# Kernel optimization log

Hardware: AMD Instinct MI355X
Metric: run time of the kernel (lower is better)

Reference implementation:

```python
import jax, jax.numpy as jnp
import numpy as np

GRID = 128      # voxel grid extent per axis
NUM_BATCH = 4
N_PER = 25000   # points per scene (unique voxels)
C = 128
K = 32          # number of classes in probs
HEADS = 8
SCALE = 1.0


def setup_inputs() -> dict:
    key = jax.random.key(0)
    ks = jax.random.split(key, 12)
    N = NUM_BATCH * N_PER
    # unique voxel coordinates per scene (submanifold conv assumes no duplicate sites)
    coords_list = []
    for b in range(NUM_BATCH):
        flat = jax.random.permutation(jax.random.fold_in(ks[0], b), GRID ** 3)[:N_PER]
        xyz = jnp.stack([flat // (GRID * GRID), (flat // GRID) % GRID, flat % GRID], axis=1)
        bcol = jnp.full((N_PER, 1), b)
        coords_list.append(jnp.concatenate([bcol, xyz], axis=1))
    coords = jnp.concatenate(coords_list, axis=0).astype(jnp.int32)  # [N,4] = (b,x,y,z)
    feats = jax.random.normal(ks[1], (N, C), jnp.float32)
    probs = jax.random.normal(ks[2], (N, K), jnp.float32)
    conv_w = jax.random.normal(ks[3], (27, C, C), jnp.float32) * (1.0 / np.sqrt(27 * C))
    bn_gamma = 1.0 + 0.1 * jax.random.normal(ks[4], (C,), jnp.float32)
    bn_beta = 0.1 * jax.random.normal(ks[5], (C,), jnp.float32)
    in_proj_w = jax.random.normal(ks[6], (3 * C, C), jnp.float32) / np.sqrt(C)
    in_proj_b = 0.01 * jax.random.normal(ks[7], (3 * C,), jnp.float32)
    out_proj_w = jax.random.normal(ks[8], (C, C), jnp.float32) / np.sqrt(C)
    out_proj_b = 0.01 * jax.random.normal(ks[9], (C,), jnp.float32)
    bottleneck_w = jax.random.normal(ks[10], (C, 2 * C), jnp.float32) / np.sqrt(2 * C)
    return {"feats": feats, "probs": probs, "conv_w": conv_w, "bn_gamma": bn_gamma,
            "bn_beta": bn_beta, "in_proj_w": in_proj_w, "in_proj_b": in_proj_b,
            "out_proj_w": out_proj_w, "out_proj_b": out_proj_b,
            "bottleneck_w": bottleneck_w, "coords": coords, "batch_size": NUM_BATCH}


def _subm_conv3x3(feats, coords, conv_w, batch_size):
    """Submanifold 3x3x3 sparse conv: outputs only at active sites, gathering active neighbors."""
    N = feats.shape[0]
    b, xyz = coords[:, 0], coords[:, 1:]
    grid = jnp.full((batch_size, GRID, GRID, GRID), -1, jnp.int32)
    grid = grid.at[b, xyz[:, 0], xyz[:, 1], xyz[:, 2]].set(jnp.arange(N, dtype=jnp.int32))
    out = jnp.zeros((N, conv_w.shape[-1]), feats.dtype)
    kidx = 0
    for dx in (-1, 0, 1):
        for dy in (-1, 0, 1):
            for dz in (-1, 0, 1):
                nb = xyz + jnp.array([dx, dy, dz], jnp.int32)
                inb = jnp.all((nb >= 0) & (nb < GRID), axis=1)
                nbc = jnp.clip(nb, 0, GRID - 1)
                j = grid[b, nbc[:, 0], nbc[:, 1], nbc[:, 2]]
                ok = inb & (j >= 0)
                g = jnp.where(ok[:, None], feats[jnp.maximum(j, 0)], 0.0)
                out = out + g @ conv_w[kidx]
                kidx += 1
    return out


def _forward(feats, probs, conv_w, bn_gamma, bn_beta, in_proj_w, in_proj_b,
             out_proj_w, out_proj_b, bottleneck_w, coords, batch_size):
    N, Cc = feats.shape
    dh = Cc // HEADS
    b = coords[:, 0]
    # transform_input: SubMConv3d -> BatchNorm1d (batch stats) -> ReLU
    x = _subm_conv3x3(feats, coords, conv_w, batch_size)
    mu = jnp.mean(x, axis=0)
    var = jnp.var(x, axis=0)
    x = jax.nn.relu((x - mu) * jax.lax.rsqrt(var + 1e-5) * bn_gamma + bn_beta)
    # SpatialGatherModule: per-scene softmax over points, soft-weighted context [B,K,C]
    m = b[None, :] == jnp.arange(batch_size, dtype=b.dtype)[:, None]          # [B,N]
    neg = jnp.finfo(x.dtype).min
    z = jnp.where(m[:, :, None], (SCALE * probs)[None], neg)                  # [B,N,K]
    w = jax.nn.softmax(z, axis=1)
    ctx = jnp.einsum('bnk,nc->bkc', w, x)                                     # [B,K,C]
    # per-scene MultiheadAttention (unbatched): query = points, key/value = context
    Wq, Wk, Wv = in_proj_w[:Cc], in_proj_w[Cc:2 * Cc], in_proj_w[2 * Cc:]
    bq, bk, bv = in_proj_b[:Cc], in_proj_b[Cc:2 * Cc], in_proj_b[2 * Cc:]
    q = ((x @ Wq.T + bq) * (dh ** -0.5)).reshape(N, HEADS, dh)
    kh = (ctx @ Wk.T + bk).reshape(batch_size, -1, HEADS, dh)
    vh = (ctx @ Wv.T + bv).reshape(batch_size, -1, HEADS, dh)
    scores = jnp.einsum('nhd,bkhd->nbhk', q, kh)
    scores = scores[jnp.arange(N), b]                                         # [N,H,K] pick own scene
    attn = jax.nn.softmax(scores, axis=-1)
    o = jnp.einsum('nhk,bkhd->nbhd', attn, vh)[jnp.arange(N), b]              # [N,H,dh]
    attn_out = o.reshape(N, Cc) @ out_proj_w.T + out_proj_b
    # torch code aliases feats with inputs.features, so the in-place scatter makes
    # both halves of the concat equal to attn_out (literal forward semantics)
    y = jnp.concatenate([attn_out, attn_out], axis=1) @ bottleneck_w.T
    return y


def reference(feats, probs, conv_w, bn_gamma, bn_beta, in_proj_w, in_proj_b,
              out_proj_w, out_proj_b, bottleneck_w, coords, batch_size):
    return _forward(feats, probs, conv_w, bn_gamma, bn_beta, in_proj_w, in_proj_b,
                    out_proj_w, out_proj_b, bottleneck_w, coords, batch_size)
```

## Files before the change

### kernel.cpp

```cpp
#include <hip/hip_runtime.h>
#include <hip/hip_bf16.h>

typedef __attribute__((ext_vector_type(8))) short short8;
typedef __attribute__((ext_vector_type(4))) float floatx4;

#define NB 4
#define GRIDD 128
#define GRID3 (128*128*128)
#define C 128
#define KSLOT 32
#define CTX_BPB 256
#define DEN_BLK 1024
#define STAT_BLK 1024
#define PCAP 8192

static __device__ __forceinline__ unsigned short f2bf(float f){
  unsigned u = __builtin_bit_cast(unsigned, f);
  unsigned r = (u + 0x7FFFu + ((u >> 16) & 1u)) >> 16;
  return (unsigned short)r;
}
static __device__ __forceinline__ float bf2f(unsigned short h){
  unsigned u = ((unsigned)h) << 16;
  return __builtin_bit_cast(float, u);
}

__global__ void prepk(const float* __restrict__ feats, const float* __restrict__ convw,
                      const float* __restrict__ inw,
                      unsigned short* __restrict__ Fb, unsigned short* __restrict__ Wt,
                      unsigned short* __restrict__ Wq, unsigned short* __restrict__ WkvT,
                      long total1)
{
  const long stride = (long)gridDim.x * blockDim.x;
  const long i0 = (long)blockIdx.x * blockDim.x + threadIdx.x;
  const long q4 = total1 >> 2;
  const float4* f4 = reinterpret_cast<const float4*>(feats);
  ushort4* fb4 = reinterpret_cast<ushort4*>(Fb);
  for (long i = i0; i < q4; i += stride){
    const float4 v = f4[i];
    ushort4 o; o.x = f2bf(v.x); o.y = f2bf(v.y); o.z = f2bf(v.z); o.w = f2bf(v.w);
    fb4[i] = o;
  }
  for (long i = i0; i < 27L*C*C; i += stride){
    long k = i >> 14; long r = (i >> 7) & 127; long c = i & 127;
    Wt[i] = f2bf(convw[(k << 14) + (c << 7) + r]);
  }
  for (long i = i0; i < C*C; i += stride) Wq[i] = f2bf(inw[i]);
  for (long i = i0; i < 2L*C*C; i += stride){
    long which = i >> 14, rem = i & 16383, ii = rem >> 7, cout = rem & 127;
    WkvT[i] = f2bf(inw[((1 + which) << 14) + (cout << 7) + ii]);
  }
}

__global__ __launch_bounds__(128) void w2k(const float* __restrict__ bw,
                                           const float* __restrict__ outw,
                                           const float* __restrict__ outb,
                                           unsigned short* __restrict__ W2b,
                                           float* __restrict__ b2){
  const int o = blockIdx.x, i = threadIdx.x;
  __shared__ float wcf[128];
  __shared__ float red[128];
  const float w_i = bw[(size_t)o*256 + i] + bw[(size_t)o*256 + 128 + i];
  wcf[i] = w_i;
  red[i] = w_i * outb[i];
  __syncthreads();
  float acc = 0.f;
  #pragma unroll 8
  for (int j = 0; j < 128; j++) acc = fmaf(wcf[j], outw[j*128 + i], acc);
  W2b[o*128 + i] = f2bf(acc);
  for (int s = 64; s > 0; s >>= 1){
    if (i < s) red[i] += red[i + s];
    __syncthreads();
  }
  if (i == 0) b2[o] = red[0];
}

__global__ void scatterk(const int* __restrict__ coords, int* __restrict__ gh, int N){
  int p = blockIdx.x * 256 + threadIdx.x;
  if (p < N){
    int4 cr = *reinterpret_cast<const int4*>(coords + (size_t)p * 4);
    gh[(((cr.x*GRIDD + cr.y)*GRIDD + cr.z)*GRIDD) + cr.w] = p;
  }
}

__global__ __launch_bounds__(256) void pairk(const int* __restrict__ coords,
                                             const int* __restrict__ gh,
                                             int2* __restrict__ pairs,
                                             int* __restrict__ gcnt, int N){
  __shared__ int wcnt[4][27];
  __shared__ int woff[4][27];
  const int t = threadIdx.x, wave = t >> 6, lane = t & 63;
  const int p = blockIdx.x * 256 + t;
  const bool active = p < N;
  int4 cr = make_int4(0, 0, 0, 0);
  if (active) cr = *reinterpret_cast<const int4*>(coords + (size_t)p * 4);
  const int b = cr.x, x = cr.y, y = cr.z, z = cr.w;
  int jl[27];
  #pragma unroll
  for (int k = 0; k < 27; k++){
    jl[k] = -1;
    if (k == 13) continue;
    if (active){
      const int dx = k / 9 - 1, dy = (k / 3) % 3 - 1, dz = k % 3 - 1;
      const int nx = x + dx, ny = y + dy, nz = z + dz;
      if (((unsigned)nx < 128u) & ((unsigned)ny < 128u) & ((unsigned)nz < 128u)){
        const int gi = ((((b << 7) + nx) << 7) + ny) * GRIDD + nz;
        const int jj = gh[gi];
        if ((unsigned)jj < (unsigned)N){
          const int4 cj = *reinterpret_cast<const int4*>(coords + (size_t)jj * 4);
          if (cj.x == b && cj.y == nx && cj.z == ny && cj.w == nz) jl[k] = jj;
        }
      }
    }
  }
  #pragma unroll
  for (int k = 0; k < 27; k++){
    const unsigned long long m = __ballot(jl[k] >= 0);
    if (lane == 0) wcnt[wave][k] = (int)__popcll(m);
  }
  __syncthreads();
  if (t < 27){
    const int c0 = wcnt[0][t], c1 = wcnt[1][t], c2 = wcnt[2][t], c3 = wcnt[3][t];
    const int tot = c0 + c1 + c2 + c3;
    int gb = 0;
    if (t != 13 && tot > 0) gb = atomicAdd(&gcnt[t], tot);
    woff[0][t] = gb;
    woff[1][t] = gb + c0;
    woff[2][t] = gb + c0 + c1;
    woff[3][t] = gb + c0 + c1 + c2;
  }
  __syncthreads();
  const unsigned long long ltm = ((unsigned long long)1 << lane) - 1;
  #pragma unroll
  for (int k = 0; k < 27; k++){
    if (k == 13) continue;
    const unsigned long long m = __ballot(jl[k] >= 0);
    if (jl[k] >= 0){
      const int slot = woff[wave][k] + (int)__popcll(m & ltm);
      if (slot < PCAP) pairs[(size_t)k * PCAP + slot] = make_int2(p, jl[k]);
    }
  }
}

__global__ __launch_bounds__(256) void scatk(
    const unsigned short* __restrict__ F, const unsigned short* __restrict__ Wt,
    const int2* __restrict__ pairs, const int* __restrict__ gcnt,
    float* __restrict__ X, int N)
{
  __shared__ unsigned short wl[128 * 136];
  const int k = (blockIdx.x < 13) ? blockIdx.x : blockIdx.x + 1;
  const int t = threadIdx.x;
  const unsigned short* wg = Wt + (size_t)k * C * C;
  for (int idx = t; idx < 128 * 16; idx += 256){
    const int row = idx >> 4, seg = idx & 15;
    *reinterpret_cast<short8*>(&wl[row * 136 + seg * 8]) =
        *reinterpret_cast<const short8*>(wg + row * 128 + seg * 8);
  }
  __syncthreads();
  const int cnt = min(gcnt[k], PCAP);
  const int nch = (cnt + 15) >> 4;
  const int wave = t >> 6, lane = t & 63, lo = lane & 15, hi = lane >> 4;
  for (int c = blockIdx.y * 4 + wave; c < nch; c += 32 * 4){
    const int pidx = c * 16 + lo;
    const bool pv = pidx < cnt;
    const int2 pr = pv ? pairs[(size_t)k * PCAP + pidx] : make_int2(0, 0);
    const unsigned short* frow = F + (size_t)pr.y * C;
    short8 a[4];
    #pragma unroll
    for (int kc = 0; kc < 4; kc++){
      a[kc] = *reinterpret_cast<const short8*>(frow + kc * 32 + hi * 8);
      if (!pv) a[kc] = (short8){0,0,0,0,0,0,0,0};
    }
    floatx4 acc[8];
    #pragma unroll
    for (int i = 0; i < 8; i++) acc[i] = (floatx4){0.f,0.f,0.f,0.f};
    #pragma unroll
    for (int kc = 0; kc < 4; kc++){
      const int koff = kc * 32 + hi * 8;
      #pragma unroll
      for (int ct = 0; ct < 8; ct++){
        const short8 b = *reinterpret_cast<const short8*>(&wl[(ct*16 + lo) * 136 + koff]);
        acc[ct] = __builtin_amdgcn_mfma_f32_16x16x32_bf16(a[kc], b, acc[ct], 0, 0, 0);
      }
    }
    #pragma unroll
    for (int i2 = 0; i2 < 4; i2++){
      const int src = hi * 4 + i2;
      const int row = __shfl(pr.x, src);
      if (c * 16 + src < cnt){
        #pragma unroll
        for (int ct = 0; ct < 8; ct++)
          atomicAdd(&X[(size_t)row * C + ct * 16 + lo], acc[ct][i2]);
      }
    }
  }
}

__global__ __launch_bounds__(256) void denomk(const float* __restrict__ probs,
                                              const int* __restrict__ coords,
                                              float* __restrict__ dpart, int N){
  const int t = threadIdx.x, k = t & 31, rh = t >> 5;
  float a0 = 0.f, a1 = 0.f, a2 = 0.f, a3 = 0.f;
  for (int r = blockIdx.x * 8 + rh; r < N; r += DEN_BLK * 8){
    const int b = coords[(size_t)r * 4];
    const float e = __expf(probs[(size_t)r * 32 + k]);
    a0 += (b == 0) ? e : 0.f;
    a1 += (b == 1) ? e : 0.f;
    a2 += (b == 2) ? e : 0.f;
    a3 += (b == 3) ? e : 0.f;
  }
  __shared__ float ls[8][128];
  ls[rh][0*32 + k] = a0; ls[rh][1*32 + k] = a1;
  ls[rh][2*32 + k] = a2; ls[rh][3*32 + k] = a3;
  __syncthreads();
  if (t < 128){
    float s = 0.f;
    #pragma unroll
    for (int j = 0; j < 8; j++) s += ls[j][t];
    dpart[(size_t)blockIdx.x * 128 + t] = s;
  }
}

__global__ __launch_bounds__(256) void statsk(const float* __restrict__ X,
                                              float* __restrict__ spgs, int N){
  const int t = threadIdx.x, c4 = t & 31, rg = t >> 5;
  float s0=0.f,s1=0.f,s2=0.f,s3=0.f, q0=0.f,q1=0.f,q2=0.f,q3=0.f;
  for (int r = blockIdx.x * 8 + rg; r < N; r += STAT_BLK * 8){
    const float4 v = *reinterpret_cast<const float4*>(X + (size_t)r * C + c4 * 4);
    s0 += v.x; s1 += v.y; s2 += v.z; s3 += v.w;
    q0 = fmaf(v.x, v.x, q0); q1 = fmaf(v.y, v.y, q1);
    q2 = fmaf(v.z, v.z, q2); q3 = fmaf(v.w, v.w, q3);
  }
  __shared__ float ls[256][4], lq[256][4];
  ls[t][0]=s0; ls[t][1]=s1; ls[t][2]=s2; ls[t][3]=s3;
  lq[t][0]=q0; lq[t][1]=q1; lq[t][2]=q2; lq[t][3]=q3;
  __syncthreads();
  if (t < 32){
    float as[4]={0.f,0.f,0.f,0.f}, aq[4]={0.f,0.f,0.f,0.f};
    #pragma unroll
    for (int g = 0; g < 8; g++){
      #pragma unroll
      for (int j = 0; j < 4; j++){ as[j] += ls[g*32 + t][j]; aq[j] += lq[g*32 + t][j]; }
    }
    #pragma unroll
    for (int j = 0; j < 4; j++){
      spgs[(size_t)blockIdx.x * 256 + t*4 + j] = as[j];
      spgs[(size_t)blockIdx.x * 256 + 128 + t*4 + j] = aq[j];
    }
  }
}

__global__ __launch_bounds__(128) void reduk(const float* __restrict__ pgs,
                                             const float* __restrict__ dpart,
                                             float* __restrict__ gsum,
                                             float* __restrict__ gsq,
                                             float* __restrict__ denom){
  const int which = blockIdx.x, slice = blockIdx.y, t = threadIdx.x;
  float s = 0.f;
  if (which < 2){
    const float* src = pgs + which * 128 + t;
    for (int j = slice; j < STAT_BLK; j += 8) s += src[(size_t)j * 256];
    atomicAdd((which ? gsq : gsum) + t, s);
  } else {
    const float* src = dpart + t;
    for (int j = slice; j < DEN_BLK; j += 8) s += src[(size_t)j * 128];
    atomicAdd(denom + t, s);
  }
}

__global__ void finalizek(const float* __restrict__ sums, const float* __restrict__ sumsq,
                          const float* __restrict__ gamma, const float* __restrict__ beta,
                          const float* __restrict__ denom,
                          float* __restrict__ scalev, float* __restrict__ shiftv,
                          float* __restrict__ invden, int N){
  const int t = threadIdx.x;
  const float invN = 1.f / (float)N;
  const float mu = sums[t] * invN;
  const float var = sumsq[t] * invN - mu * mu;
  const float sc = gamma[t] * rsqrtf(var + 1e-5f);
  scalev[t] = sc;
  shiftv[t] = beta[t] - mu * sc;
  invden[t] = 1.f / denom[t];
}

__global__ __launch_bounds__(256) void ctx2k(const float* __restrict__ Xm,
                                             const float* __restrict__ probs,
                                             const float* __restrict__ scalev,
                                             const float* __restrict__ shiftv,
                                             float* __restrict__ pbuf, int NPER){
  __shared__ float xL[32 * 128];
  __shared__ float pe[32 * 32];
  __shared__ float red[2 * KSLOT * C];
  const int blk = blockIdx.x;
  const int b = blk >> 8, j = blk & 255;
  const int rows = (NPER + CTX_BPB - 1) / CTX_BPB;
  const int r0 = j * rows;
  const int r1 = min(r0 + rows, NPER);
  const int t = threadIdx.x, c = t & 127, rh = t >> 7;
  const float sc = scalev[c], sh = shiftv[c];
  float acc[KSLOT];
  #pragma unroll
  for (int k = 0; k < KSLOT; k++) acc[k] = 0.f;

  for (int base = r0; base < r1; base += 32){
    __syncthreads();
    #pragma unroll
    for (int i = 0; i < 4; i++){
      const int idx = i * 256 + t;
      const int r = idx >> 5, c4 = idx & 31;
      const int rr = base + r;
      float4 v = make_float4(0.f, 0.f, 0.f, 0.f);
      if (rr < r1) v = *reinterpret_cast<const float4*>(Xm + ((size_t)b * NPER + rr) * C + c4 * 4);
      *reinterpret_cast<float4*>(&xL[r * 128 + c4 * 4]) = v;
    }
    {
      const int r = t >> 3, k4 = t & 7;
      const int rr = base + r;
      float4 v = make_float4(0.f, 0.f, 0.f, 0.f);
      if (rr < r1){
        const float4 pv = *reinterpret_cast<const float4*>(probs + ((size_t)b * NPER + rr) * 32 + k4 * 4);
        v.x = __expf(pv.x); v.y = __expf(pv.y); v.z = __expf(pv.z); v.w = __expf(pv.w);
      }
      *reinterpret_cast<float4*>(&pe[r * 32 + k4 * 4]) = v;
    }
    __syncthreads();
    const int rend = min(32, r1 - base);
    for (int r = rh; r < rend; r += 2){
      const float xv = fmaxf(fmaf(xL[r * 128 + c], sc, sh), 0.f);
      const float4* wr = reinterpret_cast<const float4*>(&pe[r * 32]);
      #pragma unroll
      for (int kq = 0; kq < 8; kq++){
        const float4 w4 = wr[kq];
        acc[kq*4+0] = fmaf(w4.x, xv, acc[kq*4+0]);
        acc[kq*4+1] = fmaf(w4.y, xv, acc[kq*4+1]);
        acc[kq*4+2] = fmaf(w4.z, xv, acc[kq*4+2]);
        acc[kq*4+3] = fmaf(w4.w, xv, acc[kq*4+3]);
      }
    }
  }
  __syncthreads();
  #pragma unroll
  for (int k = 0; k < KSLOT; k++) red[(rh * KSLOT + k) * C + c] = acc[k];
  __syncthreads();
  float* dst = pbuf + (size_t)blk * KSLOT * C;
  for (int i = t; i < KSLOT * C; i += 256) dst[i] = red[i] + red[KSLOT * C + i];
}

__global__ __launch_bounds__(256) void kvk(const float* __restrict__ pbuf,
                                           const float* __restrict__ invden,
                                           const unsigned short* __restrict__ WkvT,
                                           const float* __restrict__ inb,
                                           float* __restrict__ kh, float* __restrict__ vh){
  __shared__ float rowp[2][C];
  __shared__ float row[C];
  const int bk = blockIdx.x;
  const int b = bk >> 5, k = bk & 31;
  const int t = threadIdx.x, c = t & 127, jh = t >> 7;
  float s = 0.f;
  for (int j = jh; j < CTX_BPB; j += 2)
    s += pbuf[((size_t)(b * CTX_BPB + j) * KSLOT + k) * C + c];
  rowp[jh][c] = s;
  __syncthreads();
  if (t < C) row[t] = (rowp[0][t] + rowp[1][t]) * invden[b * KSLOT + k];
  __syncthreads();
  const int which = t >> 7;
  const unsigned short* W = WkvT + (size_t)which * C * C;
  float acc = inb[(1 + which) * C + c];
  #pragma unroll 8
  for (int i = 0; i < C; i++) acc = fmaf(row[i], bf2f(W[i * C + c]), acc);
  (which ? vh : kh)[(size_t)bk * C + c] = acc;
}

__global__ __launch_bounds__(256) void gemm128(
    const unsigned short* __restrict__ A, const unsigned short* __restrict__ W,
    const float* __restrict__ bias, float scale,
    float* __restrict__ outF, unsigned short* __restrict__ outB, int N)
{
  const int tid = threadIdx.x;
  const int wave = tid >> 6, lane = tid & 63;
  const int rbase = blockIdx.x * 64 + (wave >> 1) * 32;
  const int cbase = (wave & 1) * 64;
  const int lo = lane & 15, hi = lane >> 4;
  floatx4 acc[2][4];
  #pragma unroll
  for (int rt = 0; rt < 2; rt++)
    #pragma unroll
    for (int ct = 0; ct < 4; ct++) acc[rt][ct] = (floatx4){0.f,0.f,0.f,0.f};
  const int m0 = rbase + lo, m1 = rbase + 16 + lo;
  const int m0c = m0 < N ? m0 : N - 1;
  const int m1c = m1 < N ? m1 : N - 1;
  #pragma unroll
  for (int kc = 0; kc < 4; kc++){
    const int koff = kc * 32 + hi * 8;
    const short8 a0 = *reinterpret_cast<const short8*>(A + (size_t)m0c * C + koff);
    const short8 a1 = *reinterpret_cast<const short8*>(A + (size_t)m1c * C + koff);
    #pragma unroll
    for (int ct = 0; ct < 4; ct++){
      const int n = cbase + ct * 16 + lo;
      const short8 b = *reinterpret_cast<const short8*>(W + (size_t)n * C + koff);
      acc[0][ct] = __builtin_amdgcn_mfma_f32_16x16x32_bf16(a0, b, acc[0][ct], 0, 0, 0);
      acc[1][ct] = __builtin_amdgcn_mfma_f32_16x16x32_bf16(a1, b, acc[1][ct], 0, 0, 0);
    }
  }
  #pragma unroll
  for (int rt = 0; rt < 2; rt++){
    #pragma unroll
    for (int ct = 0; ct < 4; ct++){
      const int col = cbase + ct * 16 + lo;
      const float bv = bias ? bias[col] : 0.f;
      #pragma unroll
      for (int i = 0; i < 4; i++){
        const int row = rbase + rt * 16 + hi * 4 + i;
        if (row < N){
          const float v = (acc[rt][ct][i] + bv) * scale;
          if (outF) outF[(size_t)row * C + col] = v;
          if (outB) outB[(size_t)row * C + col] = f2bf(v);
        }
      }
    }
  }
}

__global__ __launch_bounds__(256) void gemm128f(
    const float* __restrict__ A, const unsigned short* __restrict__ W,
    const float* __restrict__ bias, const float* __restrict__ bnsc,
    const float* __restrict__ bnsh, float scale,
    unsigned short* __restrict__ outB, int N)
{
  const int tid = threadIdx.x;
  const int wave = tid >> 6, lane = tid & 63;
  const int rbase = blockIdx.x * 64 + (wave >> 1) * 32;
  const int cbase = (wave & 1) * 64;
  const int lo = lane & 15, hi = lane >> 4;
  floatx4 acc[2][4];
  #pragma unroll
  for (int rt = 0; rt < 2; rt++)
    #pragma unroll
    for (int ct = 0; ct < 4; ct++) acc[rt][ct] = (floatx4){0.f,0.f,0.f,0.f};
  const int m0 = rbase + lo, m1 = rbase + 16 + lo;
  const int m0c = m0 < N ? m0 : N - 1;
  const int m1c = m1 < N ? m1 : N - 1;
  #pragma unroll
  for (int kc = 0; kc < 4; kc++){
    const int koff = kc * 32 + hi * 8;
    short8 a0, a1;
    #pragma unroll
    for (int half = 0; half < 2; half++){
      const float4 sc = *reinterpret_cast<const float4*>(bnsc + koff + half * 4);
      const float4 sh = *reinterpret_cast<const float4*>(bnsh + koff + half * 4);
      const float4 x0 = *reinterpret_cast<const float4*>(A + (size_t)m0c * C + koff + half * 4);
      const float4 x1 = *reinterpret_cast<const float4*>(A + (size_t)m1c * C + koff + half * 4);
      const float* scp = &sc.x; const float* shp = &sh.x;
      const float* x0p = &x0.x; const float* x1p = &x1.x;
      #pragma unroll
      for (int j = 0; j < 4; j++){
        a0[half*4 + j] = (short)f2bf(fmaxf(fmaf(x0p[j], scp[j], shp[j]), 0.f));
        a1[half*4 + j] = (short)f2bf(fmaxf(fmaf(x1p[j], scp[j], shp[j]), 0.f));
      }
    }
    #pragma unroll
    for (int ct = 0; ct < 4; ct++){
      const int n = cbase + ct * 16 + lo;
      const short8 b = *reinterpret_cast<const short8*>(W + (size_t)n * C + koff);
      acc[0][ct] = __builtin_amdgcn_mfma_f32_16x16x32_bf16(a0, b, acc[0][ct], 0, 0, 0);
      acc[1][ct] = __builtin_amdgcn_mfma_f32_16x16x32_bf16(a1, b, acc[1][ct], 0, 0, 0);
    }
  }
  #pragma unroll
  for (int rt = 0; rt < 2; rt++){
    #pragma unroll
    for (int ct = 0; ct < 4; ct++){
      const int col = cbase + ct * 16 + lo;
      const float bv = bias[col];
      #pragma unroll
      for (int i = 0; i < 4; i++){
        const int row = rbase + rt * 16 + hi * 4 + i;
        if (row < N) outB[(size_t)row * C + col] = f2bf((acc[rt][ct][i] + bv) * scale);
      }
    }
  }
}

__global__ __launch_bounds__(256) void attn3k(const unsigned short* __restrict__ qb,
                                              const float* __restrict__ kh,
                                              const float* __restrict__ vh,
                                              unsigned short* __restrict__ ob, int NPER){
  __shared__ float khL[KSLOT * C];
  __shared__ float vhL[KSLOT * C];
  const int t = threadIdx.x;
  const int b = blockIdx.y;
  const int n0 = blockIdx.x * 64;
  {
    const float4* ks = reinterpret_cast<const float4*>(kh + (size_t)b * KSLOT * C);
    const float4* vs = reinterpret_cast<const float4*>(vh + (size_t)b * KSLOT * C);
    float4* kd = reinterpret_cast<float4*>(khL);
    float4* vd = reinterpret_cast<float4*>(vhL);
    #pragma unroll
    for (int i = 0; i < 4; i++){ kd[i * 256 + t] = ks[i * 256 + t]; vd[i * 256 + t] = vs[i * 256 + t]; }
  }
  __syncthreads();
  const int h = t >> 5, p = t & 31;
  for (int g = 0; g < 2; g++){
    const int n = n0 + g * 32 + p;
    const int nc = n < NPER ? n : NPER - 1;
    float qv[16];
    {
      const short8* qp = reinterpret_cast<const short8*>(qb + ((size_t)b * NPER + nc) * C + h * 16);
      const short8 qa = qp[0], qc = qp[1];
      #pragma unroll
      for (int i = 0; i < 8; i++){
        qv[i]     = bf2f((unsigned short)qa[i]);
        qv[8 + i] = bf2f((unsigned short)qc[i]);
      }
    }
    float sv[KSLOT];
    #pragma unroll
    for (int k = 0; k < KSLOT; k++){
      const float4* kp = reinterpret_cast<const float4*>(&khL[k * C + h * 16]);
      const float4 k0 = kp[0], k1 = kp[1], k2 = kp[2], k3 = kp[3];
      float s;
      s = qv[0] * k0.x;
      s = fmaf(qv[1], k0.y, s);  s = fmaf(qv[2],  k0.z, s);  s = fmaf(qv[3],  k0.w, s);
      s = fmaf(qv[4], k1.x, s);  s = fmaf(qv[5],  k1.y, s);  s = fmaf(qv[6],  k1.z, s);
      s = fmaf(qv[7], k1.w, s);  s = fmaf(qv[8],  k2.x, s);  s = fmaf(qv[9],  k2.y, s);
      s = fmaf(qv[10], k2.z, s); s = fmaf(qv[11], k2.w, s);  s = fmaf(qv[12], k3.x, s);
      s = fmaf(qv[13], k3.y, s); s = fmaf(qv[14], k3.z, s);  s = fmaf(qv[15], k3.w, s);
      sv[k] = s;
    }
    float m = sv[0];
    #pragma unroll
    for (int k = 1; k < KSLOT; k++) m = fmaxf(m, sv[k]);
    float sum = 0.f;
    #pragma unroll
    for (int k = 0; k < KSLOT; k++){ const float e = __expf(sv[k] - m); sv[k] = e; sum += e; }
    const float inv = 1.f / sum;
    float o[16];
    #pragma unroll
    for (int i = 0; i < 16; i++) o[i] = 0.f;
    #pragma unroll
    for (int k = 0; k < KSLOT; k++){
      const float w = sv[k];
      const float4* vp = reinterpret_cast<const float4*>(&vhL[k * C + h * 16]);
      const float4 v0 = vp[0], v1 = vp[1], v2 = vp[2], v3 = vp[3];
      o[0]  = fmaf(w, v0.x, o[0]);  o[1]  = fmaf(w, v0.y, o[1]);
      o[2]  = fmaf(w, v0.z, o[2]);  o[3]  = fmaf(w, v0.w, o[3]);
      o[4]  = fmaf(w, v1.x, o[4]);  o[5]  = fmaf(w, v1.y, o[5]);
      o[6]  = fmaf(w, v1.z, o[6]);  o[7]  = fmaf(w, v1.w, o[7]);
      o[8]  = fmaf(w, v2.x, o[8]);  o[9]  = fmaf(w, v2.y, o[9]);
      o[10] = fmaf(w, v2.z, o[10]); o[11] = fmaf(w, v2.w, o[11]);
      o[12] = fmaf(w, v3.x, o[12]); o[13] = fmaf(w, v3.y, o[13]);
      o[14] = fmaf(w, v3.z, o[14]); o[15] = fmaf(w, v3.w, o[15]);
    }
    if (n < NPER){
      short8 s0, s1;
      #pragma unroll
      for (int i = 0; i < 8; i++){
        s0[i] = (short)f2bf(o[i] * inv);
        s1[i] = (short)f2bf(o[8 + i] * inv);
      }
      unsigned short* op = ob + ((size_t)b * NPER + n) * C + h * 16;
      *reinterpret_cast<short8*>(op) = s0;
      *reinterpret_cast<short8*>(op + 8) = s1;
    }
  }
}

extern "C" void kernel_launch(void* const* d_in, const int* in_sizes, int n_in,
                              void* d_out, int out_size, void* d_ws, size_t ws_size,
                              hipStream_t stream){
  const float* feats  = (const float*)d_in[0];
  const float* probs  = (const float*)d_in[1];
  const float* convw  = (const float*)d_in[2];
  const float* gamma  = (const float*)d_in[3];
  const float* beta   = (const float*)d_in[4];
  const float* inw    = (const float*)d_in[5];
  const float* inb    = (const float*)d_in[6];
  const float* outw   = (const float*)d_in[7];
  const float* outb   = (const float*)d_in[8];
  const float* bw     = (const float*)d_in[9];
  const int*   coords = (const int*)d_in[10];
  const int N = in_sizes[0] / C;
  const int NPER = N / NB;
  const int NBLK = (N + 63) / 64;

  char* ws = (char*)d_ws;
  size_t off = 0;
  auto alloc = [&](size_t bytes) -> char* {
    char* r = ws + off; off += (bytes + 255) & ~(size_t)255; return r;
  };
  int* grid_h            = (int*)alloc((size_t)NB * GRID3 * 4);
  unsigned short* featsb = (unsigned short*)alloc((size_t)N * C * 2);
  unsigned short* convwt = (unsigned short*)alloc((size_t)27 * C * C * 2);
  unsigned short* wq     = (unsigned short*)alloc((size_t)C * C * 2);
  unsigned short* wkvT   = (unsigned short*)alloc((size_t)2 * C * C * 2);
  unsigned short* w2b    = (unsigned short*)alloc((size_t)C * C * 2);
  float* b2              = (float*)alloc(512);
  float* xconv           = (float*)alloc((size_t)N * C * 4);
  unsigned short* qb     = (unsigned short*)alloc((size_t)N * C * 2);
  int2* pairs            = (int2*)alloc((size_t)27 * PCAP * 8);
  float* spgs            = (float*)alloc((size_t)STAT_BLK * 256 * 4);
  float* dpart           = (float*)alloc((size_t)DEN_BLK * 128 * 4);
  float* zero_base       = (float*)alloc((size_t)512 * 4);
  float* gsum   = zero_base;
  float* gsq    = zero_base + 128;
  float* denom  = zero_base + 256;
  int*   gcnt   = (int*)(zero_base + 384);
  float* invden = (float*)alloc(512);
  float* scalev = (float*)alloc(512);
  float* shiftv = (float*)alloc(512);
  float* kh     = (float*)alloc((size_t)NB * KSLOT * C * 4);
  float* vh     = (float*)alloc((size_t)NB * KSLOT * C * 4);
  float* pbuf = (float*)grid_h;
  unsigned short* o_bf = featsb;

  (void)hipMemsetAsync(zero_base, 0, (size_t)512 * 4, stream);
  prepk<<<2048, 256, 0, stream>>>(feats, convw, inw, featsb, convwt, wq, wkvT, (long)N * C);
  w2k<<<128, 128, 0, stream>>>(bw, outw, outb, w2b, b2);
  scatterk<<<(N + 255) / 256, 256, 0, stream>>>(coords, grid_h, N);
  pairk<<<(N + 255) / 256, 256, 0, stream>>>(coords, grid_h, pairs, gcnt, N);
  denomk<<<DEN_BLK, 256, 0, stream>>>(probs, coords, dpart, N);
  gemm128<<<NBLK, 256, 0, stream>>>(featsb, convwt + 13 * C * C, nullptr, 1.f, xconv, nullptr, N);
  scatk<<<dim3(26, 32), 256, 0, stream>>>(featsb, convwt, pairs, gcnt, xconv, N);
  statsk<<<STAT_BLK, 256, 0, stream>>>(xconv, spgs, N);
  {
    dim3 rg(3, 8);
    reduk<<<rg, 128, 0, stream>>>(spgs, dpart, gsum, gsq, denom);
  }
  finalizek<<<1, 128, 0, stream>>>(gsum, gsq, gamma, beta, denom, scalev, shiftv, invden, N);
  ctx2k<<<NB * CTX_BPB, 256, 0, stream>>>(xconv, probs, scalev, shiftv, pbuf, NPER);
  kvk<<<NB * KSLOT, 256, 0, stream>>>(pbuf, invden, wkvT, inb, kh, vh);
  gemm128f<<<NBLK, 256, 0, stream>>>(xconv, wq, inb, scalev, shiftv, 0.25f, qb, N);
  dim3 agrid((NPER + 63) / 64, NB);
  attn3k<<<agrid, 256, 0, stream>>>(qb, kh, vh, o_bf, NPER);
  gemm128<<<NBLK, 256, 0, stream>>>(o_bf, w2b, b2, 1.f, (float*)d_out, nullptr, N);
}
```

Before: 457.4 us.

## Transpose MFMA operands for vectorized GEMM stores; fuse two query passes in attention

Swaps the MFMA A/B operands in both 128-wide GEMM kernels so each lane holds four consecutive output columns of one row. The epilogues can then issue float4 and ushort4 stores and vector bias loads instead of scattered scalar writes. The attention kernel now processes both 32-query groups in one pass, sharing each K/V shared-memory read across two queries, and adds an occupancy hint to launch bounds. The larger register footprint of the dual-query attention could cause spills or lower occupancy.

```diff
diff --git a/kernel.cpp b/kernel.cpp
--- a/kernel.cpp
+++ b/kernel.cpp
@@ -397,23 +397,29 @@
     for (int ct = 0; ct < 4; ct++){
       const int n = cbase + ct * 16 + lo;
       const short8 b = *reinterpret_cast<const short8*>(W + (size_t)n * C + koff);
-      acc[0][ct] = __builtin_amdgcn_mfma_f32_16x16x32_bf16(a0, b, acc[0][ct], 0, 0, 0);
-      acc[1][ct] = __builtin_amdgcn_mfma_f32_16x16x32_bf16(a1, b, acc[1][ct], 0, 0, 0);
+      acc[0][ct] = __builtin_amdgcn_mfma_f32_16x16x32_bf16(b, a0, acc[0][ct], 0, 0, 0);
+      acc[1][ct] = __builtin_amdgcn_mfma_f32_16x16x32_bf16(b, a1, acc[1][ct], 0, 0, 0);
     }
   }
   #pragma unroll
   for (int rt = 0; rt < 2; rt++){
-    #pragma unroll
-    for (int ct = 0; ct < 4; ct++){
-      const int col = cbase + ct * 16 + lo;
-      const float bv = bias ? bias[col] : 0.f;
+    const int row = rbase + rt * 16 + lo;
+    if (row < N){
       #pragma unroll
-      for (int i = 0; i < 4; i++){
-        const int row = rbase + rt * 16 + hi * 4 + i;
-        if (row < N){
-          const float v = (acc[rt][ct][i] + bv) * scale;
-          if (outF) outF[(size_t)row * C + col] = v;
-          if (outB) outB[(size_t)row * C + col] = f2bf(v);
+      for (int ct = 0; ct < 4; ct++){
+        const int col = cbase + ct * 16 + hi * 4;
+        float4 bv = make_float4(0.f, 0.f, 0.f, 0.f);
+        if (bias) bv = *reinterpret_cast<const float4*>(bias + col);
+        float4 v;
+        v.x = (acc[rt][ct][0] + bv.x) * scale;
+        v.y = (acc[rt][ct][1] + bv.y) * scale;
+        v.z = (acc[rt][ct][2] + bv.z) * scale;
+        v.w = (acc[rt][ct][3] + bv.w) * scale;
+        if (outF) *reinterpret_cast<float4*>(outF + (size_t)row * C + col) = v;
+        if (outB){
+          ushort4 u;
+          u.x = f2bf(v.x); u.y = f2bf(v.y); u.z = f2bf(v.z); u.w = f2bf(v.w);
+          *reinterpret_cast<ushort4*>(outB + (size_t)row * C + col) = u;
         }
       }
     }
@@ -461,29 +467,33 @@
     for (int ct = 0; ct < 4; ct++){
       const int n = cbase + ct * 16 + lo;
       const short8 b = *reinterpret_cast<const short8*>(W + (size_t)n * C + koff);
-      acc[0][ct] = __builtin_amdgcn_mfma_f32_16x16x32_bf16(a0, b, acc[0][ct], 0, 0, 0);
-      acc[1][ct] = __builtin_amdgcn_mfma_f32_16x16x32_bf16(a1, b, acc[1][ct], 0, 0, 0);
+      acc[0][ct] = __builtin_amdgcn_mfma_f32_16x16x32_bf16(b, a0, acc[0][ct], 0, 0, 0);
+      acc[1][ct] = __builtin_amdgcn_mfma_f32_16x16x32_bf16(b, a1, acc[1][ct], 0, 0, 0);
     }
   }
   #pragma unroll
   for (int rt = 0; rt < 2; rt++){
-    #pragma unroll
-    for (int ct = 0; ct < 4; ct++){
-      const int col = cbase + ct * 16 + lo;
-      const float bv = bias[col];
+    const int row = rbase + rt * 16 + lo;
+    if (row < N){
       #pragma unroll
-      for (int i = 0; i < 4; i++){
-        const int row = rbase + rt * 16 + hi * 4 + i;
-        if (row < N) outB[(size_t)row * C + col] = f2bf((acc[rt][ct][i] + bv) * scale);
-      }
-    }
-  }
-}
-
-__global__ __launch_bounds__(256) void attn3k(const unsigned short* __restrict__ qb,
-                                              const float* __restrict__ kh,
-                                              const float* __restrict__ vh,
-                                              unsigned short* __restrict__ ob, int NPER){
+      for (int ct = 0; ct < 4; ct++){
+        const int col = cbase + ct * 16 + hi * 4;
+        const float4 bv = *reinterpret_cast<const float4*>(bias + col);
+        ushort4 u;
+        u.x = f2bf((acc[rt][ct][0] + bv.x) * scale);
+        u.y = f2bf((acc[rt][ct][1] + bv.y) * scale);
+        u.z = f2bf((acc[rt][ct][2] + bv.z) * scale);
+        u.w = f2bf((acc[rt][ct][3] + bv.w) * scale);
+        *reinterpret_cast<ushort4*>(outB + (size_t)row * C + col) = u;
+      }
+    }
+  }
+}
+
+__global__ __launch_bounds__(256, 4) void attn3k(const unsigned short* __restrict__ qb,
+                                                 const float* __restrict__ kh,
+                                                 const float* __restrict__ vh,
+                                                 unsigned short* __restrict__ ob, int NPER){
   __shared__ float khL[KSLOT * C];
   __shared__ float vhL[KSLOT * C];
   const int t = threadIdx.x;
@@ -499,68 +509,87 @@
   }
   __syncthreads();
   const int h = t >> 5, p = t & 31;
-  for (int g = 0; g < 2; g++){
-    const int n = n0 + g * 32 + p;
-    const int nc = n < NPER ? n : NPER - 1;
-    float qv[16];
-    {
-      const short8* qp = reinterpret_cast<const short8*>(qb + ((size_t)b * NPER + nc) * C + h * 16);
-      const short8 qa = qp[0], qc = qp[1];
-      #pragma unroll
-      for (int i = 0; i < 8; i++){
-        qv[i]     = bf2f((unsigned short)qa[i]);
-        qv[8 + i] = bf2f((unsigned short)qc[i]);
-      }
-    }
-    float sv[KSLOT];
-    #pragma unroll
-    for (int k = 0; k < KSLOT; k++){
-      const float4* kp = reinterpret_cast<const float4*>(&khL[k * C + h * 16]);
-      const float4 k0 = kp[0], k1 = kp[1], k2 = kp[2], k3 = kp[3];
-      float s;
-      s = qv[0] * k0.x;
-      s = fmaf(qv[1], k0.y, s);  s = fmaf(qv[2],  k0.z, s);  s = fmaf(qv[3],  k0.w, s);
-      s = fmaf(qv[4], k1.x, s);  s = fmaf(qv[5],  k1.y, s);  s = fmaf(qv[6],  k1.z, s);
-      s = fmaf(qv[7], k1.w, s);  s = fmaf(qv[8],  k2.x, s);  s = fmaf(qv[9],  k2.y, s);
-      s = fmaf(qv[10], k2.z, s); s = fmaf(qv[11], k2.w, s);  s = fmaf(qv[12], k3.x, s);
-      s = fmaf(qv[13], k3.y, s); s = fmaf(qv[14], k3.z, s);  s = fmaf(qv[15], k3.w, s);
-      sv[k] = s;
-    }
-    float m = sv[0];
-    #pragma unroll
-    for (int k = 1; k < KSLOT; k++) m = fmaxf(m, sv[k]);
-    float sum = 0.f;
-    #pragma unroll
-    for (int k = 0; k < KSLOT; k++){ const float e = __expf(sv[k] - m); sv[k] = e; sum += e; }
-    const float inv = 1.f / sum;
-    float o[16];
-    #pragma unroll
-    for (int i = 0; i < 16; i++) o[i] = 0.f;
-    #pragma unroll
-    for (int k = 0; k < KSLOT; k++){
-      const float w = sv[k];
-      const float4* vp = reinterpret_cast<const float4*>(&vhL[k * C + h * 16]);
-      const float4 v0 = vp[0], v1 = vp[1], v2 = vp[2], v3 = vp[3];
-      o[0]  = fmaf(w, v0.x, o[0]);  o[1]  = fmaf(w, v0.y, o[1]);
-      o[2]  = fmaf(w, v0.z, o[2]);  o[3]  = fmaf(w, v0.w, o[3]);
-      o[4]  = fmaf(w, v1.x, o[4]);  o[5]  = fmaf(w, v1.y, o[5]);
-      o[6]  = fmaf(w, v1.z, o[6]);  o[7]  = fmaf(w, v1.w, o[7]);
-      o[8]  = fmaf(w, v2.x, o[8]);  o[9]  = fmaf(w, v2.y, o[9]);
-      o[10] = fmaf(w, v2.z, o[10]); o[11] = fmaf(w, v2.w, o[11]);
-      o[12] = fmaf(w, v3.x, o[12]); o[13] = fmaf(w, v3.y, o[13]);
-      o[14] = fmaf(w, v3.z, o[14]); o[15] = fmaf(w, v3.w, o[15]);
-    }
-    if (n < NPER){
-      short8 s0, s1;
-      #pragma unroll
-      for (int i = 0; i < 8; i++){
-        s0[i] = (short)f2bf(o[i] * inv);
-        s1[i] = (short)f2bf(o[8 + i] * inv);
-      }
-      unsigned short* op = ob + ((size_t)b * NPER + n) * C + h * 16;
-      *reinterpret_cast<short8*>(op) = s0;
-      *reinterpret_cast<short8*>(op + 8) = s1;
-    }
+  const int na = n0 + p, nb = n0 + 32 + p;
+  const int nac = na < NPER ? na : NPER - 1;
+  const int nbc = nb < NPER ? nb : NPER - 1;
+  float qa[16], qc[16];
+  {
+    const short8* qpa = reinterpret_cast<const short8*>(qb + ((size_t)b * NPER + nac) * C + h * 16);
+    const short8* qpb = reinterpret_cast<const short8*>(qb + ((size_t)b * NPER + nbc) * C + h * 16);
+    const short8 a0 = qpa[0], a1 = qpa[1];
+    const short8 b0 = qpb[0], b1 = qpb[1];
+    #pragma unroll
+    for (int i = 0; i < 8; i++){
+      qa[i]     = bf2f((unsigned short)a0[i]);
+      qa[8 + i] = bf2f((unsigned short)a1[i]);
+      qc[i]     = bf2f((unsigned short)b0[i]);
+      qc[8 + i] = bf2f((unsigned short)b1[i]);
+    }
+  }
+  float sa[KSLOT], sb[KSLOT];
+  #pragma unroll
+  for (int k = 0; k < KSLOT; k++){
+    const float4* kp = reinterpret_cast<const float4*>(&khL[k * C + h * 16]);
+    const float4 k0 = kp[0], k1 = kp[1], k2 = kp[2], k3 = kp[3];
+    const float kr[16] = {k0.x,k0.y,k0.z,k0.w, k1.x,k1.y,k1.z,k1.w,
+                          k2.x,k2.y,k2.z,k2.w, k3.x,k3.y,k3.z,k3.w};
+    float x = 0.f, y = 0.f;
+    #pragma unroll
+    for (int j = 0; j < 16; j++){
+      x = fmaf(qa[j], kr[j], x);
+      y = fmaf(qc[j], kr[j], y);
+    }
+    sa[k] = x; sb[k] = y;
+  }
+  float ma = sa[0], mb = sb[0];
+  #pragma unroll
+  for (int k = 1; k < KSLOT; k++){ ma = fmaxf(ma, sa[k]); mb = fmaxf(mb, sb[k]); }
+  float suma = 0.f, sumb = 0.f;
+  #pragma unroll
+  for (int k = 0; k < KSLOT; k++){
+    const float ea = __expf(sa[k] - ma);
+    const float eb = __expf(sb[k] - mb);
+    sa[k] = ea; sb[k] = eb;
+    suma += ea; sumb += eb;
+  }
+  const float inva = 1.f / suma, invb = 1.f / sumb;
+  float oa[16], oc[16];
+  #pragma unroll
+  for (int i = 0; i < 16; i++){ oa[i] = 0.f; oc[i] = 0.f; }
+  #pragma unroll
+  for (int k = 0; k < KSLOT; k++){
+    const float4* vp = reinterpret_cast<const float4*>(&vhL[k * C + h * 16]);
+    const float4 v0 = vp[0], v1 = vp[1], v2 = vp[2], v3 = vp[3];
+    const float vr[16] = {v0.x,v0.y,v0.z,v0.w, v1.x,v1.y,v1.z,v1.w,
+                          v2.x,v2.y,v2.z,v2.w, v3.x,v3.y,v3.z,v3.w};
+    const float wa = sa[k], wb = sb[k];
+    #pragma unroll
+    for (int j = 0; j < 16; j++){
+      oa[j] = fmaf(wa, vr[j], oa[j]);
+      oc[j] = fmaf(wb, vr[j], oc[j]);
+    }
+  }
+  if (na < NPER){
+    short8 s0, s1;
+    #pragma unroll
+    for (int i = 0; i < 8; i++){
+      s0[i] = (short)f2bf(oa[i] * inva);
+      s1[i] = (short)f2bf(oa[8 + i] * inva);
+    }
+    unsigned short* op = ob + ((size_t)b * NPER + na) * C + h * 16;
+    *reinterpret_cast<short8*>(op) = s0;
+    *reinterpret_cast<short8*>(op + 8) = s1;
+  }
+  if (nb < NPER){
+    short8 s0, s1;
+    #pragma unroll
+    for (int i = 0; i < 8; i++){
+      s0[i] = (short)f2bf(oc[i] * invb);
+      s1[i] = (short)f2bf(oc[8 + i] * invb);
+    }
+    unsigned short* op = ob + ((size_t)b * NPER + nb) * C + h * 16;
+    *reinterpret_cast<short8*>(op) = s0;
+    *reinterpret_cast<short8*>(op + 8) = s1;
   }
 }
 
```

Result: slower. 1.690 ms (+269.5%).
